# Kernel optimization log

Measured on AMD Instinct MI355X. Metric: run time of the kernel, lower is better.

The kernel has to match this reference:

```python
import jax, jax.numpy as jnp
import numpy as np

B, NQ, NA, C, L = 8, 2048, 64, 128, 4  # batches, queries/mol, atoms/mol, hidden, num_layers
CUTOFF = 8.0
E_AQ, E_QQ = 131072, 262144


def _ln(x, g, b):
    m = x.mean(-1, keepdims=True)
    v = ((x - m) ** 2).mean(-1, keepdims=True)
    return (x - m) * jax.lax.rsqrt(v + 1e-5) * g + b


def _egnn(p, h_src, h_tgt, pos_src, pos_tgt, t_emb, esrc, etgt):
    (mW1, mb1, mW2, mb2, cW1, cb1, cW2, cb2, nW1, nb1, nW2, nb2, g, b) = p
    rel = pos_tgt[etgt] - pos_src[esrc]                      # (E,3)
    sq = (rel ** 2).sum(-1, keepdims=True)                   # (E,1)
    mi = jnp.concatenate([h_src[esrc], h_tgt[etgt], sq, t_emb[etgt]], -1)  # (E,3C+1)
    msg = jax.nn.silu(jax.nn.silu(mi @ mW1 + mb1) @ mW2 + mb2)             # (E,C)
    w = jnp.tanh(jax.nn.silu(msg @ cW1 + cb1) @ cW2 + cb2)                 # (E,1)
    vel = jnp.zeros_like(pos_tgt).at[etgt].add(w * rel)
    agg = jnp.zeros_like(h_tgt).at[etgt].add(msg)
    u = jnp.concatenate([h_tgt, agg], -1)
    h_new = _ln(h_tgt + (jax.nn.silu(u @ nW1 + nb1) @ nW2 + nb2), g, b)
    return h_new, vel


def setup_inputs() -> dict:
    key = jax.random.key(0)
    ks = iter(jax.random.split(key, 64))
    n = lambda shape, s=0.05: jax.random.normal(next(ks), shape, dtype=jnp.float32) * s
    NQT, NAT = B * NQ, B * NA
    return dict(
        x_t=jax.random.normal(next(ks), (NQT, 3), dtype=jnp.float32) * 3.0,
        t_query=jax.random.uniform(next(ks), (NQT,), dtype=jnp.float32),
        atom_pos=jax.random.normal(next(ks), (NAT, 3), dtype=jnp.float32) * 3.0,
        atom_feat=n((NAT, 256), 1.0),
        edge_aq_src=jax.random.randint(next(ks), (E_AQ,), 0, NAT, dtype=jnp.int32),
        edge_aq_tgt=jax.random.randint(next(ks), (E_AQ,), 0, NQT, dtype=jnp.int32),
        edge_qq_src=jax.random.randint(next(ks), (E_QQ,), 0, NQT, dtype=jnp.int32),
        edge_qq_tgt=jax.random.randint(next(ks), (E_QQ,), 0, NQT, dtype=jnp.int32),
        atom_proj_W=n((256, C)), atom_proj_b=jnp.zeros((C,)),
        time_W1=n((C, 4 * C)), time_b1=jnp.zeros((4 * C,)),
        time_W2=n((4 * C, C)), time_b2=jnp.zeros((C,)),
        qi_W1=n((1, C)), qi_b1=jnp.zeros((C,)),
        qi_W2=n((C, C)), qi_b2=jnp.zeros((C,)),
        msg_W1=n((2 * L, 3 * C + 1, 2 * C)), msg_b1=jnp.zeros((2 * L, 2 * C)),
        msg_W2=n((2 * L, 2 * C, C)), msg_b2=jnp.zeros((2 * L, C)),
        cw_W1=n((2 * L, C, C // 2)), cw_b1=jnp.zeros((2 * L, C // 2)),
        cw_W2=n((2 * L, C // 2, 1)), cw_b2=jnp.zeros((2 * L, 1)),
        nu_W1=n((2 * L, 2 * C, C)), nu_b1=jnp.zeros((2 * L, C)),
        nu_W2=n((2 * L, C, C)), nu_b2=jnp.zeros((2 * L, C)),
        ln_g=jnp.ones((2 * L, C)), ln_b=jnp.zeros((2 * L, C)),
        vo_W1=n((C, C)), vo_b1=jnp.zeros((C,)),
        vo_W2=n((C, 1)), vo_b2=jnp.zeros((1,)),
    )


def reference(x_t, t_query, atom_pos, atom_feat,
              edge_aq_src, edge_aq_tgt, edge_qq_src, edge_qq_tgt,
              atom_proj_W, atom_proj_b,
              time_W1, time_b1, time_W2, time_b2,
              qi_W1, qi_b1, qi_W2, qi_b2,
              msg_W1, msg_b1, msg_W2, msg_b2,
              cw_W1, cw_b1, cw_W2, cw_b2,
              nu_W1, nu_b1, nu_W2, nu_b2,
              ln_g, ln_b,
              vo_W1, vo_b1, vo_W2, vo_b2):
    # atom features (no condition drop: eval mode)
    h_atom = atom_feat @ atom_proj_W + atom_proj_b

    # sinusoidal time embedding per query node
    half = C // 2
    freqs = jnp.exp(-np.log(10000.0) * jnp.arange(half, dtype=jnp.float32) / (half - 1))
    args = t_query[:, None] * freqs[None, :]
    emb = jnp.concatenate([jnp.sin(args), jnp.cos(args)], -1)
    t_emb = jax.nn.silu(emb @ time_W1 + time_b1) @ time_W2 + time_b2

    # init query features: log1p(mean_dist / cutoff), equal-size batches
    q = x_t.reshape(B, NQ, 3)
    a = atom_pos.reshape(B, NA, 3)
    sq = ((q[:, :, None, :] - a[:, None, :, :]) ** 2).sum(-1)  # (B,NQ,NA)
    log_dist = jnp.log1p(jnp.sqrt(sq.mean(-1)) / CUTOFF).reshape(-1, 1)
    h = jax.nn.silu(log_dist @ qi_W1 + qi_b1) @ qi_W2 + qi_b2

    layers = (msg_W1, msg_b1, msg_W2, msg_b2, cw_W1, cw_b1, cw_W2, cw_b2,
              nu_W1, nu_b1, nu_W2, nu_b2, ln_g, ln_b)
    pick = lambda j: tuple(arr[j] for arr in layers)

    vel = jnp.zeros_like(x_t)
    for i in range(L):
        h, dv = _egnn(pick(2 * i), h_atom, h, atom_pos, x_t, t_emb, edge_aq_src, edge_aq_tgt)
        vel = vel + dv
        h, dv = _egnn(pick(2 * i + 1), h, h, x_t, x_t, t_emb, edge_qq_src, edge_qq_tgt)
        vel = vel + dv

    scale = jax.nn.silu(h @ vo_W1 + vo_b1) @ vo_W2 + vo_b2   # (N_q,1)
    return vel * scale
```

## Files before the change

kernel.cpp:

```cpp
#include <hip/hip_runtime.h>

#define NQT 16384
#define NAT 512
#define EAQ 131072
#define EQQ 262144

typedef short short8 __attribute__((ext_vector_type(8)));
typedef float float4v __attribute__((ext_vector_type(4)));

__device__ __forceinline__ float silu_f(float x){ return x / (1.f + __expf(-x)); }

__device__ __forceinline__ short f2bf(float f){
  union { float f; unsigned u; } v; v.f = f;
  unsigned r = v.u + 0x7fff + ((v.u >> 16) & 1);
  return (short)(r >> 16);
}
__device__ __forceinline__ float bf2f(short s){
  union { unsigned u; float f; } v;
  v.u = ((unsigned)(unsigned short)s) << 16;
  return v.f;
}

__global__ __launch_bounds__(256) void k_hist2(
    const int* __restrict__ ta, const int* __restrict__ tq,
    int* __restrict__ ha, int* __restrict__ hq)
{
  int i = blockIdx.x*256 + threadIdx.x;
  atomicAdd(&hq[tq[i]], 1);
  if (i < EAQ) atomicAdd(&ha[ta[i]], 1);
}

__global__ __launch_bounds__(256) void k_scan2(int* __restrict__ ha, int* __restrict__ hq)
{
  int* hist = (blockIdx.x == 0) ? ha : hq;
  __shared__ int part[256];
  int t = threadIdx.x;
  int base = t * 64;
  int s = 0;
  for (int i = 0; i < 64; i++) s += hist[base + i];
  part[t] = s;
  __syncthreads();
  for (int off = 1; off < 256; off <<= 1){
    int v = (t >= off) ? part[t - off] : 0;
    __syncthreads();
    part[t] += v;
    __syncthreads();
  }
  int run = (t == 0) ? 0 : part[t-1];
  for (int i = 0; i < 64; i++){
    int h = hist[base + i];
    hist[base + i] = run;
    run += h;
  }
}

__global__ __launch_bounds__(256) void k_place2(
    const int* __restrict__ sa, const int* __restrict__ ta,
    const int* __restrict__ sq, const int* __restrict__ tq,
    int* __restrict__ ca, int* __restrict__ cq,
    int2* __restrict__ da, int2* __restrict__ dq)
{
  int i = blockIdx.x*256 + threadIdx.x;
  { int tg = tq[i]; int pos = atomicAdd(&cq[tg], 1); dq[pos] = make_int2(sq[i], tg); }
  if (i < EAQ){ int tg = ta[i]; int pos = atomicAdd(&ca[tg], 1); da[pos] = make_int2(sa[i], tg); }
}

__device__ __forceinline__ void pack_one(
    const float* __restrict__ W, short* __restrict__ out,
    int rows, int cols, int ksteps, int ntiles, int idx, int mode)
{
  int l8   = idx & 7;
  int lane = (idx >> 3) & 63;
  int kk   = (idx >> 9) % ksteps;
  int nt   = ((idx >> 9) / ksteps) % ntiles;
  int j    = idx / (512 * ksteps * ntiles);
  int k = kk*32 + (lane >> 4)*8 + l8;
  if (mode == 1) k += (k >= 256);
  else if (mode == 2) k = (k < 128) ? k + 128 : k + 129;
  int n = nt*16 + (lane & 15);
  out[idx] = f2bf(W[(size_t)j*rows*cols + (size_t)k*cols + n]);
}

__global__ __launch_bounds__(256) void k_packall(
    const float* __restrict__ mW1, const float* __restrict__ mW2,
    const float* __restrict__ cW1, const float* __restrict__ nW1,
    const float* __restrict__ nW2, const float* __restrict__ tW1,
    const float* __restrict__ tW2,
    short* W1ap, short* W1bcp, short* W2p, short* W3p,
    short* nW1p, short* nW2p, short* tW1p, short* tW2p)
{
  int b = blockIdx.x, t = threadIdx.x;
  if (b < 1024){ pack_one(mW1, W1ap, 385,256,4,16, b*256+t, 0); return; } b -= 1024;
  if (b < 2048){ pack_one(mW1, W1bcp,385,256,8,16, b*256+t, 2); return; } b -= 2048;
  if (b < 1024){ pack_one(mW2, W2p,  256,128,8, 8, b*256+t, 0); return; } b -= 1024;
  if (b <  256){ pack_one(cW1, W3p,  128, 64,4, 4, b*256+t, 0); return; } b -=  256;
  if (b < 1024){ pack_one(nW1, nW1p, 256,128,8, 8, b*256+t, 0); return; } b -= 1024;
  if (b <  512){ pack_one(nW2, nW2p, 128,128,4, 8, b*256+t, 0); return; } b -=  512;
  if (b <  256){ pack_one(tW1, tW1p, 128,512,4,32, b*256+t, 0); return; } b -=  256;
  pack_one(tW2, tW2p, 512,128,16,8, b*256+t, 0);
}

__global__ __launch_bounds__(256) void k_pre0(
    const float* __restrict__ hA, const float* __restrict__ temb,
    const float* __restrict__ mb1_0, const short* __restrict__ W1bcp0,
    const float* __restrict__ h_atom, const short* __restrict__ W1ap_base,
    short* __restrict__ Ptgt, short* __restrict__ psrc_aq)
{
  int t = threadIdx.x;
  int lane = t & 63, w = t >> 6;
  int mrow = lane & 15, quad = lane >> 4;
  int b = blockIdx.x;

  if (b < NQT/64){
    int m0 = b*64 + w*16;
    short8 areg[8];
    #pragma unroll
    for (int kk = 0; kk < 8; kk++){
      int k = kk*32 + quad*8;
      const float* bp = (kk >= 4) ? (temb + (size_t)(m0+mrow)*128 + (k - 128))
                                  : (hA   + (size_t)(m0+mrow)*128 + k);
      float4 f0 = *(const float4*)(bp);
      float4 f1 = *(const float4*)(bp + 4);
      short8 s;
      s[0]=f2bf(f0.x); s[1]=f2bf(f0.y); s[2]=f2bf(f0.z); s[3]=f2bf(f0.w);
      s[4]=f2bf(f1.x); s[5]=f2bf(f1.y); s[6]=f2bf(f1.z); s[7]=f2bf(f1.w);
      areg[kk] = s;
    }
    #pragma unroll
    for (int nt = 0; nt < 16; nt++){
      float4v acc = {0.f,0.f,0.f,0.f};
      const short8* Bb = (const short8*)(W1bcp0 + ((size_t)nt*8)*512 + lane*8);
      #pragma unroll
      for (int kk = 0; kk < 8; kk++)
        acc = __builtin_amdgcn_mfma_f32_16x16x32_bf16(areg[kk], Bb[kk*64], acc, 0, 0, 0);
      float bv = mb1_0[nt*16 + mrow];
      #pragma unroll
      for (int r = 0; r < 4; r++)
        Ptgt[(size_t)(m0 + quad*4 + r)*256 + nt*16 + mrow] = f2bf(acc[r] + bv);
    }
  } else {
    int bb = b - NQT/64;
    int idx = bb >> 3;
    int m0 = (bb & 7)*64 + w*16;
    const short* Wp = W1ap_base + (size_t)(2*idx)*32768;
    short8 areg[4];
    #pragma unroll
    for (int kk = 0; kk < 4; kk++){
      const float* bp = h_atom + (size_t)(m0+mrow)*128 + kk*32 + quad*8;
      float4 f0 = *(const float4*)(bp);
      float4 f1 = *(const float4*)(bp + 4);
      short8 s;
      s[0]=f2bf(f0.x); s[1]=f2bf(f0.y); s[2]=f2bf(f0.z); s[3]=f2bf(f0.w);
      s[4]=f2bf(f1.x); s[5]=f2bf(f1.y); s[6]=f2bf(f1.z); s[7]=f2bf(f1.w);
      areg[kk] = s;
    }
    #pragma unroll
    for (int nt = 0; nt < 16; nt++){
      float4v acc = {0.f,0.f,0.f,0.f};
      const short8* Bb = (const short8*)(Wp + ((size_t)nt*4)*512 + lane*8);
      #pragma unroll
      for (int kk = 0; kk < 4; kk++)
        acc = __builtin_amdgcn_mfma_f32_16x16x32_bf16(areg[kk], Bb[kk*64], acc, 0, 0, 0);
      #pragma unroll
      for (int r = 0; r < 4; r++)
        psrc_aq[(size_t)idx*131072 + (size_t)(m0 + quad*4 + r)*256 + nt*16 + mrow] = f2bf(acc[r]);
    }
  }
}

__global__ __launch_bounds__(128) void k_hatom(
    const float* __restrict__ feat, const float* __restrict__ W,
    const float* __restrict__ b, float* __restrict__ out)
{
  __shared__ float sf[256];
  int n = blockIdx.x, t = threadIdx.x;
  sf[t]       = feat[n*256 + t];
  sf[t + 128] = feat[n*256 + 128 + t];
  __syncthreads();
  float acc = b[t];
  for (int k = 0; k < 256; k++) acc += sf[k] * W[k*128 + t];
  out[n*128 + t] = acc;
}

__global__ __launch_bounds__(256) void k_temb(
    const float* __restrict__ tq,
    const short* __restrict__ W1p, const float* __restrict__ b1,
    const short* __restrict__ W2p, const float* __restrict__ b2,
    float* __restrict__ temb)
{
  __shared__ __align__(16) short A[32*136];
  __shared__ __align__(16) short B[32*528];
  int t = threadIdx.x;
  int n0 = blockIdx.x * 32;

  {
    int row = t >> 3, l = t & 7;
    float tv = tq[n0 + row];
    short* o = A + row*136;
    #pragma unroll
    for (int i = 0; i < 16; i++){
      int k = l*16 + i;
      int h = k & 63;
      float freq = __expf(-9.210340371976184f * (float)h * (1.f/63.f));
      float a = tv * freq;
      float v = (k < 64) ? __sinf(a) : __cosf(a);
      o[k] = f2bf(v);
    }
  }
  __syncthreads();

  int lane = t & 63, w = t >> 6;
  int mrow = lane & 15, quad = lane >> 4;

  for (int nti = 0; nti < 8; nti++){
    int nt = w*8 + nti;
    #pragma unroll
    for (int mt = 0; mt < 2; mt++){
      float4v acc = {0.f,0.f,0.f,0.f};
      const short8* Ab = (const short8*)(A + (mt*16 + mrow)*136 + quad*8);
      const short8* Bb = (const short8*)(W1p + (size_t)nt*4*512 + lane*8);
      #pragma unroll
      for (int kk = 0; kk < 4; kk++)
        acc = __builtin_amdgcn_mfma_f32_16x16x32_bf16(Ab[kk*4], Bb[kk*64], acc, 0, 0, 0);
      int n = nt*16 + mrow;
      float b1n = b1[n];
      #pragma unroll
      for (int r = 0; r < 4; r++)
        B[(mt*16 + quad*4 + r)*528 + n] = f2bf(silu_f(acc[r] + b1n));
    }
  }
  __syncthreads();

  #pragma unroll
  for (int nti = 0; nti < 2; nti++){
    int nt = w*2 + nti;
    #pragma unroll
    for (int mt = 0; mt < 2; mt++){
      float4v acc = {0.f,0.f,0.f,0.f};
      const short8* Ab = (const short8*)(B + (mt*16 + mrow)*528 + quad*8);
      const short8* Bb = (const short8*)(W2p + (size_t)nt*16*512 + lane*8);
      #pragma unroll
      for (int kk = 0; kk < 16; kk++)
        acc = __builtin_amdgcn_mfma_f32_16x16x32_bf16(Ab[kk*4], Bb[kk*64], acc, 0, 0, 0);
      int n = nt*16 + mrow;
      float b2n = b2[n];
      #pragma unroll
      for (int r = 0; r < 4; r++)
        temb[(size_t)(n0 + mt*16 + quad*4 + r)*128 + n] = acc[r] + b2n;
    }
  }
}

__global__ __launch_bounds__(128) void k_hinit(
    const float* __restrict__ x_t, const float* __restrict__ atom_pos,
    const float* __restrict__ W1, const float* __restrict__ b1,
    const float* __restrict__ W2, const float* __restrict__ b2,
    float* __restrict__ h)
{
  __shared__ float sh[128];
  __shared__ float sld;
  int n = blockIdx.x, t = threadIdx.x;
  float qx = x_t[n*3], qy = x_t[n*3+1], qz = x_t[n*3+2];
  float part = 0.f;
  if (t < 64){
    int a = (n >> 11)*64 + t;
    float dx = qx - atom_pos[a*3];
    float dy = qy - atom_pos[a*3+1];
    float dz = qz - atom_pos[a*3+2];
    part = dx*dx + dy*dy + dz*dz;
  }
  #pragma unroll
  for (int off = 32; off; off >>= 1) part += __shfl_down(part, off);
  if (t == 0) sld = log1pf(sqrtf(part * (1.f/64.f)) * 0.125f);
  __syncthreads();
  float ld = sld;
  sh[t] = silu_f(ld * W1[t] + b1[t]);
  __syncthreads();
  float acc = b2[t];
  for (int k = 0; k < 128; k++) acc += sh[k] * W2[k*128 + t];
  h[(size_t)n*128 + t] = acc;
}

__global__ __launch_bounds__(256) void k_edge(
    const short* __restrict__ Psrc, const short* __restrict__ Ptgt,
    const float* __restrict__ pos_src, const float* __restrict__ pos_tgt,
    const int2* __restrict__ sdesc,
    const float* __restrict__ w1sq,
    const short* __restrict__ W2p, const float* __restrict__ b2,
    const short* __restrict__ W3p, const float* __restrict__ b3,
    const float* __restrict__ W4,  const float* __restrict__ b4,
    float* __restrict__ agg, float* __restrict__ vel)
{
  __shared__ __align__(16) short A2[32*264];
  __shared__ __align__(16) short A3[32*136];
  __shared__ float rel_s[32*3];
  __shared__ int   tgt_s[32];
  float* msgf = (float*)A2;
  float* h3   = (float*)A2;

  int t = threadIdx.x;
  int e0 = blockIdx.x * 32;

  {
    int e = t >> 3, l = t & 7;
    int2 d = sdesc[e0 + e];
    int src = d.x, tgt = d.y;
    float rx = pos_tgt[tgt*3+0] - pos_src[src*3+0];
    float ry = pos_tgt[tgt*3+1] - pos_src[src*3+1];
    float rz = pos_tgt[tgt*3+2] - pos_src[src*3+2];
    float sqv = rx*rx + ry*ry + rz*rz;
    if (l == 0){
      rel_s[e*3+0]=rx; rel_s[e*3+1]=ry; rel_s[e*3+2]=rz;
      tgt_s[e] = tgt;
    }
    const short8* ps = (const short8*)(Psrc + (size_t)src*256);
    const short8* pt = (const short8*)(Ptgt + (size_t)tgt*256);
    #pragma unroll
    for (int c = 0; c < 4; c++){
      int ci = c*8 + l;
      int n0 = ci*8;
      short8 a = ps[ci], b = pt[ci];
      float4 w0 = *(const float4*)(w1sq + n0);
      float4 w1 = *(const float4*)(w1sq + n0 + 4);
      short8 r;
      r[0] = f2bf(silu_f(bf2f(a[0]) + bf2f(b[0]) + sqv*w0.x));
      r[1] = f2bf(silu_f(bf2f(a[1]) + bf2f(b[1]) + sqv*w0.y));
      r[2] = f2bf(silu_f(bf2f(a[2]) + bf2f(b[2]) + sqv*w0.z));
      r[3] = f2bf(silu_f(bf2f(a[3]) + bf2f(b[3]) + sqv*w0.w));
      r[4] = f2bf(silu_f(bf2f(a[4]) + bf2f(b[4]) + sqv*w1.x));
      r[5] = f2bf(silu_f(bf2f(a[5]) + bf2f(b[5]) + sqv*w1.y));
      r[6] = f2bf(silu_f(bf2f(a[6]) + bf2f(b[6]) + sqv*w1.z));
      r[7] = f2bf(silu_f(bf2f(a[7]) + bf2f(b[7]) + sqv*w1.w));
      *(short8*)(A2 + e*264 + n0) = r;
    }
  }
  __syncthreads();

  int lane = t & 63, w = t >> 6;
  int mrow = lane & 15, quad = lane >> 4;

  float4v acc2[2][2];
  #pragma unroll
  for (int nti = 0; nti < 2; nti++){
    int nt = w*2 + nti;
    #pragma unroll
    for (int mt = 0; mt < 2; mt++){
      float4v acc = {0.f,0.f,0.f,0.f};
      const short8* Ab = (const short8*)(A2 + (mt*16 + mrow)*264 + quad*8);
      const short8* Bb = (const short8*)(W2p + (size_t)nt*8*512 + lane*8);
      #pragma unroll
      for (int kk = 0; kk < 8; kk++)
        acc = __builtin_amdgcn_mfma_f32_16x16x32_bf16(Ab[kk*4], Bb[kk*64], acc, 0, 0, 0);
      acc2[nti][mt] = acc;
    }
  }
  __syncthreads();

  #pragma unroll
  for (int nti = 0; nti < 2; nti++){
    int n = (w*2 + nti)*16 + mrow;
    float b2n = b2[n];
    #pragma unroll
    for (int mt = 0; mt < 2; mt++){
      #pragma unroll
      for (int r = 0; r < 4; r++){
        int e = mt*16 + quad*4 + r;
        float v = silu_f(acc2[nti][mt][r] + b2n);
        msgf[e*132 + n] = v;
        A3[e*136 + n]   = f2bf(v);
      }
    }
  }
  __syncthreads();

  float4v acc3[2];
  {
    int nt = w;
    #pragma unroll
    for (int mt = 0; mt < 2; mt++){
      float4v acc = {0.f,0.f,0.f,0.f};
      const short8* Ab = (const short8*)(A3 + (mt*16 + mrow)*136 + quad*8);
      const short8* Bb = (const short8*)(W3p + (size_t)nt*4*512 + lane*8);
      #pragma unroll
      for (int kk = 0; kk < 4; kk++)
        acc = __builtin_amdgcn_mfma_f32_16x16x32_bf16(Ab[kk*4], Bb[kk*64], acc, 0, 0, 0);
      acc3[mt] = acc;
    }
  }

  {
    int c = t & 127, hh = t >> 7;
    int eb = hh*16;
    float run = 0.f;
    int cur = tgt_s[eb];
    for (int e = eb; e < eb + 16; e++){
      int tg = tgt_s[e];
      if (tg != cur){
        atomicAdd(&agg[(size_t)cur*128 + c], run);
        run = 0.f; cur = tg;
      }
      run += msgf[e*132 + c];
    }
    atomicAdd(&agg[(size_t)cur*128 + c], run);
  }
  __syncthreads();

  {
    int n = w*16 + mrow;
    float b3n = b3[n];
    #pragma unroll
    for (int mt = 0; mt < 2; mt++){
      #pragma unroll
      for (int r = 0; r < 4; r++){
        int e = mt*16 + quad*4 + r;
        h3[e*68 + n] = silu_f(acc3[mt][r] + b3n);
      }
    }
  }
  __syncthreads();

  {
    int e = t >> 3, l = t & 7;
    float p = 0.f;
    #pragma unroll
    for (int i = 0; i < 8; i++){
      int k = l + 8*i;
      p += h3[e*68 + k] * W4[k];
    }
    p += __shfl_xor(p, 1);
    p += __shfl_xor(p, 2);
    p += __shfl_xor(p, 4);
    if (l == 0){
      float wv = tanhf(p + b4[0]);
      int tg = tgt_s[e];
      atomicAdd(&vel[tg*3+0], wv*rel_s[e*3+0]);
      atomicAdd(&vel[tg*3+1], wv*rel_s[e*3+1]);
      atomicAdd(&vel[tg*3+2], wv*rel_s[e*3+2]);
    }
  }
}

__global__ __launch_bounds__(256) void k_node(
    const float* __restrict__ h, float* __restrict__ agg,
    const short* __restrict__ W1p, const float* __restrict__ b1,
    const short* __restrict__ W2p, const float* __restrict__ b2,
    const float* __restrict__ g, const float* __restrict__ bb_,
    float* __restrict__ h_out,
    int produce,
    const float* __restrict__ temb,
    const short* __restrict__ W1bcN, const float* __restrict__ mb1N,
    const short* __restrict__ W1aN,
    short* __restrict__ Ptgt, short* __restrict__ PsrcQ)
{
  __shared__ __align__(16) short A[32*264];
  __shared__ __align__(16) short B[32*136];
  __shared__ __align__(16) short S[32*264];
  float* r = (float*)A;
  int t = threadIdx.x;
  int n0 = blockIdx.x * 32;

  {
    int row = t >> 3, l = t & 7;
    const float4* hr = (const float4*)(h + (size_t)(n0+row)*128);
    float4*       ar = (float4*)(agg + (size_t)(n0+row)*128);
    const float4* te = (const float4*)(temb + (size_t)(n0+row)*128);
    short* o = A + row*264;
    short* so = S + row*264 + 128;
    float4 z = make_float4(0.f,0.f,0.f,0.f);
    #pragma unroll
    for (int i = 0; i < 4; i++){
      int k4 = l + 8*i;
      float4 a = hr[k4];
      o[k4*4+0]=f2bf(a.x); o[k4*4+1]=f2bf(a.y); o[k4*4+2]=f2bf(a.z); o[k4*4+3]=f2bf(a.w);
      float4 b = ar[k4];
      o[128 + k4*4+0]=f2bf(b.x); o[128 + k4*4+1]=f2bf(b.y);
      o[128 + k4*4+2]=f2bf(b.z); o[128 + k4*4+3]=f2bf(b.w);
      ar[k4] = z;
      if (produce){
        float4 c = te[k4];
        so[k4*4+0]=f2bf(c.x); so[k4*4+1]=f2bf(c.y);
        so[k4*4+2]=f2bf(c.z); so[k4*4+3]=f2bf(c.w);
      }
    }
  }
  __syncthreads();

  int lane = t & 63, w = t >> 6;
  int mrow = lane & 15, quad = lane >> 4;

  float4v accA[2][2];
  #pragma unroll
  for (int nti = 0; nti < 2; nti++){
    int nt = w*2 + nti;
    #pragma unroll
    for (int mt = 0; mt < 2; mt++){
      float4v acc = {0.f,0.f,0.f,0.f};
      const short8* Ab = (const short8*)(A + (mt*16 + mrow)*264 + quad*8);
      const short8* Bb = (const short8*)(W1p + (size_t)nt*8*512 + lane*8);
      #pragma unroll
      for (int kk = 0; kk < 8; kk++)
        acc = __builtin_amdgcn_mfma_f32_16x16x32_bf16(Ab[kk*4], Bb[kk*64], acc, 0, 0, 0);
      accA[nti][mt] = acc;
    }
  }
  __syncthreads();

  #pragma unroll
  for (int nti = 0; nti < 2; nti++){
    int n = (w*2 + nti)*16 + mrow;
    float b1n = b1[n];
    #pragma unroll
    for (int mt = 0; mt < 2; mt++){
      #pragma unroll
      for (int rr = 0; rr < 4; rr++){
        int e = mt*16 + quad*4 + rr;
        B[e*136 + n] = f2bf(silu_f(accA[nti][mt][rr] + b1n));
      }
    }
  }
  __syncthreads();

  #pragma unroll
  for (int nti = 0; nti < 2; nti++){
    int nt = w*2 + nti;
    #pragma unroll
    for (int mt = 0; mt < 2; mt++){
      float4v acc = {0.f,0.f,0.f,0.f};
      const short8* Ab = (const short8*)(B + (mt*16 + mrow)*136 + quad*8);
      const short8* Bb = (const short8*)(W2p + (size_t)nt*4*512 + lane*8);
      #pragma unroll
      for (int kk = 0; kk < 4; kk++)
        acc = __builtin_amdgcn_mfma_f32_16x16x32_bf16(Ab[kk*4], Bb[kk*64], acc, 0, 0, 0);
      int n = nt*16 + mrow;
      float b2n = b2[n];
      #pragma unroll
      for (int rr = 0; rr < 4; rr++){
        int e = mt*16 + quad*4 + rr;
        r[e*132 + n] = h[(size_t)(n0+e)*128 + n] + acc[rr] + b2n;
      }
    }
  }
  __syncthreads();

  {
    int lane2 = t & 63, wid = t >> 6;
    #pragma unroll
    for (int nn = 0; nn < 8; nn++){
      int row = wid*8 + nn;
      float a = r[row*132 + lane2], bv = r[row*132 + lane2 + 64];
      float s = a + bv, ss = a*a + bv*bv;
      #pragma unroll
      for (int off = 1; off < 64; off <<= 1){
        s  += __shfl_xor(s, off);
        ss += __shfl_xor(ss, off);
      }
      float mean = s * (1.f/128.f);
      float var  = ss * (1.f/128.f) - mean*mean;
      float rstd = rsqrtf(var + 1e-5f);
      float v0 = (a  - mean)*rstd*g[lane2]      + bb_[lane2];
      float v1 = (bv - mean)*rstd*g[lane2 + 64] + bb_[lane2 + 64];
      float* ho = h_out + (size_t)(n0+row)*128;
      ho[lane2]      = v0;
      ho[lane2 + 64] = v1;
      S[row*264 + lane2]      = f2bf(v0);
      S[row*264 + lane2 + 64] = f2bf(v1);
    }
  }
  if (!produce) return;
  __syncthreads();

  #pragma unroll
  for (int nti = 0; nti < 4; nti++){
    int nt = w*4 + nti;
    #pragma unroll
    for (int mt = 0; mt < 2; mt++){
      float4v acc = {0.f,0.f,0.f,0.f};
      const short8* Ab = (const short8*)(S + (mt*16 + mrow)*264 + quad*8);
      const short8* Bb = (const short8*)(W1bcN + (size_t)nt*8*512 + lane*8);
      #pragma unroll
      for (int kk = 0; kk < 8; kk++)
        acc = __builtin_amdgcn_mfma_f32_16x16x32_bf16(Ab[kk*4], Bb[kk*64], acc, 0, 0, 0);
      int n = nt*16 + mrow;
      float bv = mb1N[n];
      #pragma unroll
      for (int rr = 0; rr < 4; rr++)
        Ptgt[(size_t)(n0 + mt*16 + quad*4 + rr)*256 + n] = f2bf(acc[rr] + bv);
    }
  }

  if (produce == 2){
    #pragma unroll
    for (int nti = 0; nti < 4; nti++){
      int nt = w*4 + nti;
      #pragma unroll
      for (int mt = 0; mt < 2; mt++){
        float4v acc = {0.f,0.f,0.f,0.f};
        const short8* Ab = (const short8*)(S + (mt*16 + mrow)*264 + quad*8);
        const short8* Bb = (const short8*)(W1aN + (size_t)nt*4*512 + lane*8);
        #pragma unroll
        for (int kk = 0; kk < 4; kk++)
          acc = __builtin_amdgcn_mfma_f32_16x16x32_bf16(Ab[kk*4], Bb[kk*64], acc, 0, 0, 0);
        int n = nt*16 + mrow;
        #pragma unroll
        for (int rr = 0; rr < 4; rr++)
          PsrcQ[(size_t)(n0 + mt*16 + quad*4 + rr)*256 + n] = f2bf(acc[rr]);
      }
    }
  }
}

__global__ __launch_bounds__(128) void k_out(
    const float* __restrict__ h, const float* __restrict__ vel,
    const float* __restrict__ W1, const float* __restrict__ b1,
    const float* __restrict__ W2, const float* __restrict__ b2,
    float* __restrict__ out)
{
  __shared__ float sh[128];
  __shared__ float spart[2];
  int n = blockIdx.x, t = threadIdx.x;
  sh[t] = h[(size_t)n*128 + t];
  __syncthreads();
  float acc = b1[t];
  for (int k = 0; k < 128; k++) acc += sh[k] * W1[k*128 + t];
  float p = silu_f(acc) * W2[t];
  #pragma unroll
  for (int off = 32; off; off >>= 1) p += __shfl_down(p, off);
  if ((t & 63) == 0) spart[t >> 6] = p;
  __syncthreads();
  if (t < 3){
    float scale = spart[0] + spart[1] + b2[0];
    out[n*3 + t] = vel[n*3 + t] * scale;
  }
}

extern "C" void kernel_launch(void* const* d_in, const int* in_sizes, int n_in,
                              void* d_out, int out_size, void* d_ws, size_t ws_size,
                              hipStream_t stream)
{
  const float* x_t       = (const float*)d_in[0];
  const float* t_query   = (const float*)d_in[1];
  const float* atom_pos  = (const float*)d_in[2];
  const float* atom_feat = (const float*)d_in[3];
  const int*   e_aq_s = (const int*)d_in[4];
  const int*   e_aq_t = (const int*)d_in[5];
  const int*   e_qq_s = (const int*)d_in[6];
  const int*   e_qq_t = (const int*)d_in[7];
  const float* apW  = (const float*)d_in[8];
  const float* apb  = (const float*)d_in[9];
  const float* tW1  = (const float*)d_in[10];
  const float* tb1  = (const float*)d_in[11];
  const float* tW2  = (const float*)d_in[12];
  const float* tb2  = (const float*)d_in[13];
  const float* qiW1 = (const float*)d_in[14];
  const float* qib1 = (const float*)d_in[15];
  const float* qiW2 = (const float*)d_in[16];
  const float* qib2 = (const float*)d_in[17];
  const float* mW1  = (const float*)d_in[18];
  const float* mb1  = (const float*)d_in[19];
  const float* mW2  = (const float*)d_in[20];
  const float* mb2  = (const float*)d_in[21];
  const float* cW1  = (const float*)d_in[22];
  const float* cb1  = (const float*)d_in[23];
  const float* cW2  = (const float*)d_in[24];
  const float* cb2  = (const float*)d_in[25];
  const float* nW1  = (const float*)d_in[26];
  const float* nb1  = (const float*)d_in[27];
  const float* nW2  = (const float*)d_in[28];
  const float* nb2  = (const float*)d_in[29];
  const float* lng  = (const float*)d_in[30];
  const float* lnb  = (const float*)d_in[31];
  const float* voW1 = (const float*)d_in[32];
  const float* vob1 = (const float*)d_in[33];
  const float* voW2 = (const float*)d_in[34];
  const float* vob2 = (const float*)d_in[35];
  float* out = (float*)d_out;

  float* ws     = (float*)d_ws;
  float* h_atom = ws;
  float* temb   = h_atom + 65536;
  float* hA     = temb + 2097152;
  float* hB     = hA + 2097152;
  float* agg    = hB + 2097152;
  float* vel    = agg + 2097152;
  short* W1ap   = (short*)(vel + 49152);
  short* W1bcp  = W1ap + 262144;
  short* W2p    = W1bcp + 524288;
  short* W3p    = W2p + 262144;
  short* nW1p   = W3p + 65536;
  short* nW2p   = nW1p + 262144;
  short* tW1p   = nW2p + 131072;
  short* tW2p   = tW1p + 65536;
  short* PsrcQ  = tW2p + 65536;
  short* Ptgt   = PsrcQ + 4194304;
  short* psrc_aq= Ptgt + 4194304;
  int*   hist_a = (int*)(psrc_aq + 524288);
  int*   hist_q = hist_a + 16384;
  int2*  desc_a = (int2*)(hist_q + 16384);
  int2*  desc_q = desc_a + EAQ;

  hipMemsetAsync(hist_a, 0, 2*16384*sizeof(int), stream);
  k_hist2<<<EQQ/256, 256, 0, stream>>>(e_aq_t, e_qq_t, hist_a, hist_q);
  k_scan2<<<2, 256, 0, stream>>>(hist_a, hist_q);
  k_place2<<<EQQ/256, 256, 0, stream>>>(e_aq_s, e_aq_t, e_qq_s, e_qq_t,
                                        hist_a, hist_q, desc_a, desc_q);

  k_packall<<<6400, 256, 0, stream>>>(mW1, mW2, cW1, nW1, nW2, tW1, tW2,
      W1ap, W1bcp, W2p, W3p, nW1p, nW2p, tW1p, tW2p);

  hipMemsetAsync(agg, 0, (size_t)(NQT*128 + NQT*3)*sizeof(float), stream);
  k_hatom<<<NAT, 128, 0, stream>>>(atom_feat, apW, apb, h_atom);
  k_temb<<<NQT/32, 256, 0, stream>>>(t_query, tW1p, tb1, tW2p, tb2, temb);
  k_hinit<<<NQT, 128, 0, stream>>>(x_t, atom_pos, qiW1, qib1, qiW2, qib2, hA);

  k_pre0<<<NQT/64 + 32, 256, 0, stream>>>(hA, temb, mb1, W1bcp, h_atom, W1ap,
                                          Ptgt, psrc_aq);

  float* hc = hA; float* hn = hB;
  for (int j = 0; j < 8; j++){
    int half = j & 1;
    const int2* dsc = half ? desc_q : desc_a;
    int E = half ? EQQ : EAQ;
    const short* psrc = half ? PsrcQ : (psrc_aq + (size_t)(j >> 1)*131072);

    k_edge<<<E/32, 256, 0, stream>>>(psrc, Ptgt,
        half ? x_t : atom_pos, x_t, dsc,
        mW1 + (size_t)j*385*256 + 65536,
        W2p + (size_t)j*32768, mb2 + (size_t)j*128,
        W3p + (size_t)j*8192,  cb1 + (size_t)j*64,
        cW2 + (size_t)j*64,    cb2 + (size_t)j,
        agg, vel);

    int jn = (j < 7) ? (j + 1) : 7;
    int produce = (j == 7) ? 0 : ((half == 0) ? 2 : 1);
    k_node<<<NQT/32, 256, 0, stream>>>(hc, agg,
        nW1p + (size_t)j*32768, nb1 + (size_t)j*128,
        nW2p + (size_t)j*16384, nb2 + (size_t)j*128,
        lng + (size_t)j*128,    lnb + (size_t)j*128, hn,
        produce, temb,
        W1bcp + (size_t)jn*65536, mb1 + (size_t)jn*256,
        W1ap + (size_t)jn*32768,
        Ptgt, PsrcQ);
    float* tmp = hc; hc = hn; hn = tmp;
  }
  k_out<<<NQT, 128, 0, stream>>>(hc, vel, voW1, vob1, voW2, vob2, out);
}
```

Baseline: 1.318 ms.

## Keep edge-MLP A fragments in registers and process 64 edges per block

The edge kernel now has each wavefront own 16 edges and build its first-layer bf16 A fragments directly in registers, feeding MFMA without staging through shared memory. The block tile grows from 32 to 64 edges, and each wave computes all output tiles of the second and third layers for its own rows. The bf16 copy of the message is rebuilt from the fp32 shared buffer, so one shared array and a barrier go away. In exchange, register pressure rises (8 A fragments plus 8 accumulators), each wave now reads every weight tile, and the launch has half as many blocks.

Result: slower. 1.373 ms (+4.2%).

```diff
diff --git a/kernel.cpp b/kernel.cpp
--- a/kernel.cpp
+++ b/kernel.cpp
@@ -291,37 +291,39 @@
     const float* __restrict__ W4,  const float* __restrict__ b4,
     float* __restrict__ agg, float* __restrict__ vel)
 {
-  __shared__ __align__(16) short A2[32*264];
-  __shared__ __align__(16) short A3[32*136];
-  __shared__ float rel_s[32*3];
-  __shared__ int   tgt_s[32];
-  float* msgf = (float*)A2;
-  float* h3   = (float*)A2;
+  __shared__ float msgf[64*132];
+  __shared__ float rel_s[64*3];
+  __shared__ int   tgt_s[64];
+  float* h3 = msgf;
 
   int t = threadIdx.x;
-  int e0 = blockIdx.x * 32;
-
+  int lane = t & 63, w = t >> 6;
+  int mrow = lane & 15, quad = lane >> 4;
+  int e0 = blockIdx.x * 64;
+
+  int eMine = e0 + w*16 + mrow;
+  int2 d = sdesc[eMine];
+  int src = d.x, tgt = d.y;
+  float rx = pos_tgt[tgt*3+0] - pos_src[src*3+0];
+  float ry = pos_tgt[tgt*3+1] - pos_src[src*3+1];
+  float rz = pos_tgt[tgt*3+2] - pos_src[src*3+2];
+  float sqv = rx*rx + ry*ry + rz*rz;
+  if (quad == 0){
+    int le = w*16 + mrow;
+    tgt_s[le] = tgt;
+    rel_s[le*3+0]=rx; rel_s[le*3+1]=ry; rel_s[le*3+2]=rz;
+  }
+
+  short8 afrag[8];
   {
-    int e = t >> 3, l = t & 7;
-    int2 d = sdesc[e0 + e];
-    int src = d.x, tgt = d.y;
-    float rx = pos_tgt[tgt*3+0] - pos_src[src*3+0];
-    float ry = pos_tgt[tgt*3+1] - pos_src[src*3+1];
-    float rz = pos_tgt[tgt*3+2] - pos_src[src*3+2];
-    float sqv = rx*rx + ry*ry + rz*rz;
-    if (l == 0){
-      rel_s[e*3+0]=rx; rel_s[e*3+1]=ry; rel_s[e*3+2]=rz;
-      tgt_s[e] = tgt;
-    }
     const short8* ps = (const short8*)(Psrc + (size_t)src*256);
     const short8* pt = (const short8*)(Ptgt + (size_t)tgt*256);
     #pragma unroll
-    for (int c = 0; c < 4; c++){
-      int ci = c*8 + l;
-      int n0 = ci*8;
+    for (int kk = 0; kk < 8; kk++){
+      int ci = kk*4 + quad;
       short8 a = ps[ci], b = pt[ci];
-      float4 w0 = *(const float4*)(w1sq + n0);
-      float4 w1 = *(const float4*)(w1sq + n0 + 4);
+      float4 w0 = *(const float4*)(w1sq + ci*8);
+      float4 w1 = *(const float4*)(w1sq + ci*8 + 4);
       short8 r;
       r[0] = f2bf(silu_f(bf2f(a[0]) + bf2f(b[0]) + sqv*w0.x));
       r[1] = f2bf(silu_f(bf2f(a[1]) + bf2f(b[1]) + sqv*w0.y));
@@ -331,69 +333,63 @@
       r[5] = f2bf(silu_f(bf2f(a[5]) + bf2f(b[5]) + sqv*w1.y));
       r[6] = f2bf(silu_f(bf2f(a[6]) + bf2f(b[6]) + sqv*w1.z));
       r[7] = f2bf(silu_f(bf2f(a[7]) + bf2f(b[7]) + sqv*w1.w));
-      *(short8*)(A2 + e*264 + n0) = r;
-    }
-  }
-  __syncthreads();
-
-  int lane = t & 63, w = t >> 6;
-  int mrow = lane & 15, quad = lane >> 4;
-
-  float4v acc2[2][2];
-  #pragma unroll
-  for (int nti = 0; nti < 2; nti++){
-    int nt = w*2 + nti;
-    #pragma unroll
-    for (int mt = 0; mt < 2; mt++){
+      afrag[kk] = r;
+    }
+  }
+
+  float4v acc2[8];
+  #pragma unroll
+  for (int nt = 0; nt < 8; nt++){
+    float4v acc = {0.f,0.f,0.f,0.f};
+    const short8* Bb = (const short8*)(W2p + (size_t)nt*8*512 + lane*8);
+    #pragma unroll
+    for (int kk = 0; kk < 8; kk++)
+      acc = __builtin_amdgcn_mfma_f32_16x16x32_bf16(afrag[kk], Bb[kk*64], acc, 0, 0, 0);
+    acc2[nt] = acc;
+  }
+
+  #pragma unroll
+  for (int nt = 0; nt < 8; nt++){
+    int n = nt*16 + mrow;
+    float b2n = b2[n];
+    #pragma unroll
+    for (int r = 0; r < 4; r++){
+      int e = w*16 + quad*4 + r;
+      msgf[e*132 + n] = silu_f(acc2[nt][r] + b2n);
+    }
+  }
+  __syncthreads();
+
+  float4v acc3[4];
+  {
+    short8 a3[4];
+    #pragma unroll
+    for (int kk = 0; kk < 4; kk++){
+      const float* mp = msgf + (size_t)(w*16 + mrow)*132 + kk*32 + quad*8;
+      float4 f0 = *(const float4*)(mp);
+      float4 f1 = *(const float4*)(mp + 4);
+      short8 s;
+      s[0]=f2bf(f0.x); s[1]=f2bf(f0.y); s[2]=f2bf(f0.z); s[3]=f2bf(f0.w);
+      s[4]=f2bf(f1.x); s[5]=f2bf(f1.y); s[6]=f2bf(f1.z); s[7]=f2bf(f1.w);
+      a3[kk] = s;
+    }
+    #pragma unroll
+    for (int nt = 0; nt < 4; nt++){
       float4v acc = {0.f,0.f,0.f,0.f};
-      const short8* Ab = (const short8*)(A2 + (mt*16 + mrow)*264 + quad*8);
-      const short8* Bb = (const short8*)(W2p + (size_t)nt*8*512 + lane*8);
-      #pragma unroll
-      for (int kk = 0; kk < 8; kk++)
-        acc = __builtin_amdgcn_mfma_f32_16x16x32_bf16(Ab[kk*4], Bb[kk*64], acc, 0, 0, 0);
-      acc2[nti][mt] = acc;
-    }
-  }
-  __syncthreads();
-
-  #pragma unroll
-  for (int nti = 0; nti < 2; nti++){
-    int n = (w*2 + nti)*16 + mrow;
-    float b2n = b2[n];
-    #pragma unroll
-    for (int mt = 0; mt < 2; mt++){
-      #pragma unroll
-      for (int r = 0; r < 4; r++){
-        int e = mt*16 + quad*4 + r;
-        float v = silu_f(acc2[nti][mt][r] + b2n);
-        msgf[e*132 + n] = v;
-        A3[e*136 + n]   = f2bf(v);
-      }
-    }
-  }
-  __syncthreads();
-
-  float4v acc3[2];
-  {
-    int nt = w;
-    #pragma unroll
-    for (int mt = 0; mt < 2; mt++){
-      float4v acc = {0.f,0.f,0.f,0.f};
-      const short8* Ab = (const short8*)(A3 + (mt*16 + mrow)*136 + quad*8);
       const short8* Bb = (const short8*)(W3p + (size_t)nt*4*512 + lane*8);
       #pragma unroll
       for (int kk = 0; kk < 4; kk++)
-        acc = __builtin_amdgcn_mfma_f32_16x16x32_bf16(Ab[kk*4], Bb[kk*64], acc, 0, 0, 0);
-      acc3[mt] = acc;
+        acc = __builtin_amdgcn_mfma_f32_16x16x32_bf16(a3[kk], Bb[kk*64], acc, 0, 0, 0);
+      acc3[nt] = acc;
     }
   }
 
   {
     int c = t & 127, hh = t >> 7;
-    int eb = hh*16;
+    int eb = hh*32;
     float run = 0.f;
     int cur = tgt_s[eb];
-    for (int e = eb; e < eb + 16; e++){
+    for (int e = eb; e < eb + 32; e++){
       int tg = tgt_s[e];
       if (tg != cur){
         atomicAdd(&agg[(size_t)cur*128 + c], run);
@@ -405,31 +401,28 @@
   }
   __syncthreads();
 
+  #pragma unroll
+  for (int nt = 0; nt < 4; nt++){
+    int n = nt*16 + mrow;
+    float b3n = b3[n];
+    #pragma unroll
+    for (int r = 0; r < 4; r++){
+      int e = w*16 + quad*4 + r;
+      h3[e*68 + n] = silu_f(acc3[nt][r] + b3n);
+    }
+  }
+  __syncthreads();
+
   {
-    int n = w*16 + mrow;
-    float b3n = b3[n];
-    #pragma unroll
-    for (int mt = 0; mt < 2; mt++){
-      #pragma unroll
-      for (int r = 0; r < 4; r++){
-        int e = mt*16 + quad*4 + r;
-        h3[e*68 + n] = silu_f(acc3[mt][r] + b3n);
-      }
-    }
-  }
-  __syncthreads();
-
-  {
-    int e = t >> 3, l = t & 7;
+    int e = t >> 2, l = t & 3;
     float p = 0.f;
     #pragma unroll
-    for (int i = 0; i < 8; i++){
-      int k = l + 8*i;
+    for (int i = 0; i < 16; i++){
+      int k = l + 4*i;
       p += h3[e*68 + k] * W4[k];
     }
     p += __shfl_xor(p, 1);
     p += __shfl_xor(p, 2);
-    p += __shfl_xor(p, 4);
     if (l == 0){
       float wv = tanhf(p + b4[0]);
       int tg = tgt_s[e];
@@ -722,7 +715,7 @@
     int E = half ? EQQ : EAQ;
     const short* psrc = half ? PsrcQ : (psrc_aq + (size_t)(j >> 1)*131072);
 
-    k_edge<<<E/32, 256, 0, stream>>>(psrc, Ptgt,
+    k_edge<<<E/64, 256, 0, stream>>>(psrc, Ptgt,
         half ? x_t : atom_pos, x_t, dsc,
         mW1 + (size_t)j*385*256 + 65536,
         W2p + (size_t)j*32768, mb2 + (size_t)j*128,
```
